# Performance work log

Hardware: AMD Instinct MI355X
Metric: run time of the kernel (lower is better)

Reference implementation:

```python
import jax, jax.numpy as jnp
import numpy as np

E, S, Q, NN_NODES, R = 2048, 256, 25, 36, 15
H = 128  # MLP hidden width


def setup_inputs() -> dict:
    key = jax.random.key(0)
    ks = jax.random.split(key, 16)
    g = lambda k, shape, scale=1.0: (jax.random.normal(k, shape, dtype=jnp.float32) * scale)
    inp = {
        "nodes": g(ks[0], (E, NN_NODES, 2)),
        "W1": g(ks[1], (2, H), 1.0 / np.sqrt(2.0)),
        "b1": jnp.zeros((H,), jnp.float32),
        "W2": g(ks[2], (H, H), 1.0 / np.sqrt(H)),
        "b2": jnp.zeros((H,), jnp.float32),
        "W3": g(ks[3], (H, H), 1.0 / np.sqrt(H)),
        "b3": jnp.zeros((H,), jnp.float32),
        "W4": g(ks[4], (H, 1), 1.0 / np.sqrt(H)),
        "b4": jnp.zeros((1,), jnp.float32),
        # 2nd-derivative interpolation matrices of the inter basis B at the
        # sub-element quadrature points (shared across big elements).
        "Ixx": g(ks[5], (S, Q, NN_NODES), 0.1),
        "Iyy": g(ks[6], (S, Q, NN_NODES), 0.1),
        # per-big-element 2x2 Hessian change-of-coordinates map (B_DD_inter)
        "B_DD": g(ks[7], (E, 2, 2)),
        "w_quad": jax.random.uniform(ks[8], (Q,), dtype=jnp.float32),
        # test-function values at quadrature points (b.Base)
        "Base": g(ks[9], (Q, R)),
        # per-sub-element Jacobians and precomputed RHS projections F_total
        "J": jax.random.uniform(ks[10], (E, S), dtype=jnp.float32),
        "F": g(ks[11], (E, S, R)),
    }
    return inp


def _mlp(x, W1, b1, W2, b2, W3, b3, W4, b4):
    h = jnp.tanh(x @ W1 + b1)
    h = jnp.tanh(h @ W2 + b2)
    h = jnp.tanh(h @ W3 + b3)
    return h @ W4 + b4


def reference(nodes, W1, b1, W2, b2, W3, b3, W4, b4,
              Ixx, Iyy, B_DD, w_quad, Base, J, F):
    # NN evaluated once per big element at its interpolation nodes: [E, n_nodes]
    ev = _mlp(nodes.reshape(-1, 2), W1, b1, W2, b2, W3, b3, W4, b4)
    ev = ev.reshape(E, NN_NODES)
    d2x = jnp.einsum("sqn,en->esq", Ixx, ev)
    d2y = jnp.einsum("sqn,en->esq", Iyy, ev)
    grad_second = jnp.stack([d2x, d2y], axis=2)           # [E,S,2,Q]
    # B_DD_inter @ grad_second^T, per big element
    grad_second = jnp.einsum("eij,esjq->esiq", B_DD, grad_second)
    integrand_1 = grad_second.sum(axis=2)                 # [E,S,Q]
    # u_NN_el[r] = -J * sum_q w[q] * Base[q,r] * integrand_1[q]
    u_el = -J[:, :, None] * jnp.einsum("q,qr,esq->esr", w_quad, Base, integrand_1)
    res = u_el - F                                        # [E,S,R]
    # loss_element = mean over test functions, summed over all (big, sub) elements
    return jnp.sum(jnp.mean(jnp.square(res), axis=-1))
```

## Files before the change

### kernel.cpp

```cpp
#include <hip/hip_runtime.h>

#define EN 2048
#define SN 256
#define QN 25
#define NNODES 36
#define RN 15
#define HN 128
#define KP 96
#define NTOT (SN * RN)

typedef __attribute__((ext_vector_type(8))) short short8;
typedef __attribute__((ext_vector_type(4))) float f32x4;
typedef __attribute__((ext_vector_type(2))) unsigned int uint2v;

__device__ __forceinline__ unsigned short f2bf(float f) {
    unsigned int u = __float_as_uint(f);
    u += 0x7fffu + ((u >> 16) & 1u);
    return (unsigned short)(u >> 16);
}
__device__ __forceinline__ float bf2f(unsigned short h) {
    return __uint_as_float(((unsigned int)h) << 16);
}
__device__ __forceinline__ float fast_tanh(float x) {
    float xs = x * 2.885390082f;
    xs = fminf(fmaxf(xs, -60.f), 60.f);
    float e = __builtin_amdgcn_exp2f(xs);
    float r = __builtin_amdgcn_rcpf(e + 1.f);
    return fmaf(-2.f, r, 1.f);
}

__device__ __forceinline__ void load_W(const float* __restrict__ W,
                                       unsigned short (*Ws)[136], int t)
{
    const int n = t & 127;
    const int h = t >> 7;
    #pragma unroll
    for (int kk = 0; kk < 16; kk++) {
        const int k0 = (kk * 2 + h) * 4;
        const float a0 = W[(k0 + 0) * HN + n];
        const float a1 = W[(k0 + 1) * HN + n];
        const float a2 = W[(k0 + 2) * HN + n];
        const float a3 = W[(k0 + 3) * HN + n];
        uint2v pk;
        pk[0] = (unsigned)f2bf(a0) | ((unsigned)f2bf(a1) << 16);
        pk[1] = (unsigned)f2bf(a2) | ((unsigned)f2bf(a3) << 16);
        *(uint2v*)&Ws[n][k0] = pk;
    }
}

__device__ __forceinline__ void mfma_layer(unsigned short (*Hs)[136],
                                           const unsigned short (*Ws)[136],
                                           const float* __restrict__ bias,
                                           int wv, int rowA, int quad)
{
    const int r0 = wv * 32;
    short8 afrag[2][4];
    #pragma unroll
    for (int rt = 0; rt < 2; rt++)
        #pragma unroll
        for (int kt = 0; kt < 4; kt++)
            afrag[rt][kt] = *(const short8*)&Hs[r0 + rt * 16 + rowA][kt * 32 + quad * 8];

    f32x4 acc[2][8];
    const f32x4 zero = {0.f, 0.f, 0.f, 0.f};
    #pragma unroll
    for (int rt = 0; rt < 2; rt++)
        #pragma unroll
        for (int nt = 0; nt < 8; nt++) acc[rt][nt] = zero;

    #pragma unroll
    for (int nt = 0; nt < 8; nt++) {
        #pragma unroll
        for (int kt = 0; kt < 4; kt++) {
            const short8 bfrag = *(const short8*)&Ws[nt * 16 + rowA][kt * 32 + quad * 8];
            acc[0][nt] = __builtin_amdgcn_mfma_f32_16x16x32_bf16(afrag[0][kt], bfrag, acc[0][nt], 0, 0, 0);
            acc[1][nt] = __builtin_amdgcn_mfma_f32_16x16x32_bf16(afrag[1][kt], bfrag, acc[1][nt], 0, 0, 0);
        }
    }
    #pragma unroll
    for (int nt = 0; nt < 8; nt++) {
        const int col = nt * 16 + rowA;
        const float bv = bias[col];
        #pragma unroll
        for (int rt = 0; rt < 2; rt++) {
            #pragma unroll
            for (int rg = 0; rg < 4; rg++) {
                const float v = fast_tanh(acc[rt][nt][rg] + bv);
                Hs[r0 + rt * 16 + quad * 4 + rg][col] = f2bf(v);
            }
        }
    }
}

#define MLP_BLOCKS 576
#define MC_BLOCKS 1440

__global__ __launch_bounds__(256, 2)
void prep_kernel(const float* __restrict__ nodes,
                 const float* __restrict__ W1, const float* __restrict__ b1,
                 const float* __restrict__ W2, const float* __restrict__ b2,
                 const float* __restrict__ W3, const float* __restrict__ b3,
                 const float* __restrict__ W4, const float* __restrict__ b4,
                 const float* __restrict__ B_DD,
                 const float* __restrict__ Ixx, const float* __restrict__ Iyy,
                 const float* __restrict__ wq, const float* __restrict__ Base,
                 unsigned short* __restrict__ evcb,
                 unsigned short* __restrict__ Mcb,
                 float* __restrict__ out)
{
    __shared__ unsigned short Hs[128][136];
    __shared__ unsigned short Ws[128][136];
    __shared__ float WB[QN * 16];
    const int bid = blockIdx.x;
    const int t   = threadIdx.x;

    if (bid < MLP_BLOCKS) {
        const int lane = t & 63;
        const int wv   = t >> 6;
        const int rowA = lane & 15;
        const int quad = lane >> 4;

        {
            const int p  = t >> 1;
            const int P  = bid * 128 + p;
            const float x0 = nodes[2 * P], x1 = nodes[2 * P + 1];
            const int n0 = (t & 1) * 64;
            #pragma unroll
            for (int i = 0; i < 16; i++) {
                const int n = n0 + 4 * i;
                const float4 wa = *(const float4*)(W1 + n);
                const float4 wb = *(const float4*)(W1 + HN + n);
                const float4 bb = *(const float4*)(b1 + n);
                const float h0 = fast_tanh(fmaf(x0, wa.x, fmaf(x1, wb.x, bb.x)));
                const float h1 = fast_tanh(fmaf(x0, wa.y, fmaf(x1, wb.y, bb.y)));
                const float h2 = fast_tanh(fmaf(x0, wa.z, fmaf(x1, wb.z, bb.z)));
                const float h3 = fast_tanh(fmaf(x0, wa.w, fmaf(x1, wb.w, bb.w)));
                uint2v pk;
                pk[0] = (unsigned)f2bf(h0) | ((unsigned)f2bf(h1) << 16);
                pk[1] = (unsigned)f2bf(h2) | ((unsigned)f2bf(h3) << 16);
                *(uint2v*)&Hs[p][n] = pk;
            }
        }
        load_W(W2, Ws, t);
        __syncthreads();
        mfma_layer(Hs, Ws, b2, wv, rowA, quad);
        __syncthreads();
        load_W(W3, Ws, t);
        __syncthreads();
        mfma_layer(Hs, Ws, b3, wv, rowA, quad);
        {
            const int p  = t >> 1;
            const int k0 = (t & 1) * 64;
            float d = 0.f;
            #pragma unroll
            for (int i = 0; i < 8; i++) {
                const short8 h = *(const short8*)&Hs[p][k0 + 8 * i];
                const float4 wA = *(const float4*)(W4 + k0 + 8 * i);
                const float4 wB = *(const float4*)(W4 + k0 + 8 * i + 4);
                d = fmaf(bf2f((unsigned short)h[0]), wA.x, d);
                d = fmaf(bf2f((unsigned short)h[1]), wA.y, d);
                d = fmaf(bf2f((unsigned short)h[2]), wA.z, d);
                d = fmaf(bf2f((unsigned short)h[3]), wA.w, d);
                d = fmaf(bf2f((unsigned short)h[4]), wB.x, d);
                d = fmaf(bf2f((unsigned short)h[5]), wB.y, d);
                d = fmaf(bf2f((unsigned short)h[6]), wB.z, d);
                d = fmaf(bf2f((unsigned short)h[7]), wB.w, d);
            }
            d += __shfl_xor(d, 1, 64);
            if ((t & 1) == 0) {
                const float ev = d + b4[0];
                const int P  = bid * 128 + p;
                const int e  = P / NNODES;
                const int ne = P - e * NNODES;
                const float c0 = B_DD[4 * e + 0] + B_DD[4 * e + 2];
                const float c1 = B_DD[4 * e + 1] + B_DD[4 * e + 3];
                evcb[e * KP + ne]          = f2bf(c0 * ev);
                evcb[e * KP + NNODES + ne] = f2bf(c1 * ev);
                if (ne < KP - 2 * NNODES)
                    evcb[e * KP + 2 * NNODES + ne] = 0;
            }
        }
    } else {
        if (bid == MLP_BLOCKS && t == 0) out[0] = 0.f;
        for (int i = t; i < QN * 16; i += 256) {
            const int q = i >> 4, r = i & 15;
            if (r < RN) WB[i] = wq[q] * Base[q * RN + r];
        }
        __syncthreads();
        const int o = (bid - MLP_BLOCKS) * 256 + t;
        const int c = o % KP;
        const int n = o / KP;
        if (c >= 2 * NNODES) { Mcb[o] = 0; return; }
        const int r = n % RN;
        const int s = n / RN;
        const float* __restrict__ I = (c < NNODES) ? Ixx : Iyy;
        const int cn = (c < NNODES) ? c : (c - NNODES);
        float a0 = 0.f, a1 = 0.f;
        #pragma unroll
        for (int q = 0; q < QN - 1; q += 2) {
            a0 = fmaf(WB[q * 16 + r],       I[(s * QN + q) * NNODES + cn],     a0);
            a1 = fmaf(WB[(q + 1) * 16 + r], I[(s * QN + q + 1) * NNODES + cn], a1);
        }
        a0 = fmaf(WB[(QN - 1) * 16 + r], I[(s * QN + QN - 1) * NNODES + cn], a0);
        Mcb[o] = f2bf(a0 + a1);
    }
}

__global__ __launch_bounds__(256, 4)
void loss_kernel(const unsigned short* __restrict__ evcb,
                 const unsigned short* __restrict__ Mcb,
                 const float* __restrict__ J, const float* __restrict__ F,
                 float* __restrict__ out)
{
    const int t    = threadIdx.x;
    const int lane = t & 63;
    const int wv   = t >> 6;
    const int rowA = lane & 15;
    const int quad = lane >> 4;
    const int m0 = (blockIdx.x & 31) * 64;
    const int n0 = (blockIdx.x >> 5) * 128 + wv * 32;

    f32x4 acc[4][2];
    const f32x4 zero = {0.f, 0.f, 0.f, 0.f};
    #pragma unroll
    for (int mt = 0; mt < 4; mt++)
        #pragma unroll
        for (int nt = 0; nt < 2; nt++) acc[mt][nt] = zero;

    #pragma unroll
    for (int kt = 0; kt < 3; kt++) {
        short8 a[4], b[2];
        #pragma unroll
        for (int mt = 0; mt < 4; mt++)
            a[mt] = *(const short8*)&evcb[(m0 + mt * 16 + rowA) * KP + kt * 32 + quad * 8];
        #pragma unroll
        for (int nt = 0; nt < 2; nt++)
            b[nt] = *(const short8*)&Mcb[(n0 + nt * 16 + rowA) * KP + kt * 32 + quad * 8];
        #pragma unroll
        for (int mt = 0; mt < 4; mt++)
            #pragma unroll
            for (int nt = 0; nt < 2; nt++)
                acc[mt][nt] = __builtin_amdgcn_mfma_f32_16x16x32_bf16(a[mt], b[nt], acc[mt][nt], 0, 0, 0);
    }

    float total = 0.f;
    #pragma unroll
    for (int nt = 0; nt < 2; nt++) {
        const int n = n0 + nt * 16 + rowA;
        const int s = (n * 34953) >> 19;
        #pragma unroll
        for (int mt = 0; mt < 4; mt++) {
            const int eb = m0 + mt * 16 + quad * 4;
            #pragma unroll
            for (int rg = 0; rg < 4; rg++) {
                const int e = eb + rg;
                const float Jv = J[e * SN + s];
                const float Fv = F[e * NTOT + n];
                const float d  = acc[mt][nt][rg];
                const float res = fmaf(-Jv, d, -Fv);
                total = fmaf(res, res, total);
            }
        }
    }
    total *= (1.f / (float)RN);

    #pragma unroll
    for (int off = 32; off; off >>= 1)
        total += __shfl_down(total, off, 64);
    __shared__ float wsum[4];
    if (lane == 0) wsum[wv] = total;
    __syncthreads();
    if (t == 0) atomicAdd(out, (wsum[0] + wsum[1]) + (wsum[2] + wsum[3]));
}

extern "C" void kernel_launch(void* const* d_in, const int* in_sizes, int n_in,
                              void* d_out, int out_size, void* d_ws, size_t ws_size,
                              hipStream_t stream)
{
    (void)in_sizes; (void)n_in; (void)out_size; (void)ws_size;
    const float* nodes = (const float*)d_in[0];
    const float* W1   = (const float*)d_in[1];
    const float* b1   = (const float*)d_in[2];
    const float* W2   = (const float*)d_in[3];
    const float* b2   = (const float*)d_in[4];
    const float* W3   = (const float*)d_in[5];
    const float* b3   = (const float*)d_in[6];
    const float* W4   = (const float*)d_in[7];
    const float* b4   = (const float*)d_in[8];
    const float* Ixx  = (const float*)d_in[9];
    const float* Iyy  = (const float*)d_in[10];
    const float* B_DD = (const float*)d_in[11];
    const float* wq   = (const float*)d_in[12];
    const float* Base = (const float*)d_in[13];
    const float* J    = (const float*)d_in[14];
    const float* F    = (const float*)d_in[15];
    float* out = (float*)d_out;
    unsigned short* evcb = (unsigned short*)d_ws;
    unsigned short* Mcb  = (unsigned short*)((char*)d_ws + EN * KP * 2);

    prep_kernel<<<MLP_BLOCKS + MC_BLOCKS, 256, 0, stream>>>(
        nodes, W1, b1, W2, b2, W3, b3, W4, b4, B_DD, Ixx, Iyy, wq, Base,
        evcb, Mcb, out);
    loss_kernel<<<32 * 30, 256, 0, stream>>>(evcb, Mcb, J, F, out);
}
```

Before: 154.1 us.

## Stage Ixx/Iyy per sub-element in LDS and prefetch F before MFMA loop

The M-matrix construction now uses one block per sub-element instead of one thread per output. Each block stages that sub-element's Ixx/Iyy slices into shared memory and reuses them across all test functions, rather than rereading them from global memory for every output. The loss kernel also loads its F values into registers before the MFMA loop so their latency overlaps the matrix compute. The cost is fewer M-construction blocks with more serial work each, and higher register pressure in the loss kernel.

```diff
diff --git a/kernel.cpp b/kernel.cpp
--- a/kernel.cpp
+++ b/kernel.cpp
@@ -93,7 +93,7 @@
 }
 
 #define MLP_BLOCKS 576
-#define MC_BLOCKS 1440
+#define MC_BLOCKS  SN
 
 __global__ __launch_bounds__(256, 2)
 void prep_kernel(const float* __restrict__ nodes,
@@ -181,28 +181,38 @@
             }
         }
     } else {
-        if (bid == MLP_BLOCKS && t == 0) out[0] = 0.f;
+        const int s = bid - MLP_BLOCKS;
+        if (s == 0 && t == 0) out[0] = 0.f;
+        float* I_lds = (float*)&Hs[0][0];
         for (int i = t; i < QN * 16; i += 256) {
             const int q = i >> 4, r = i & 15;
             if (r < RN) WB[i] = wq[q] * Base[q * RN + r];
         }
+        const float* __restrict__ Ia = Ixx + (size_t)s * (QN * NNODES);
+        const float* __restrict__ Ib = Iyy + (size_t)s * (QN * NNODES);
+        for (int i = t; i < QN * NNODES; i += 256) {
+            I_lds[i]               = Ia[i];
+            I_lds[QN * NNODES + i] = Ib[i];
+        }
         __syncthreads();
-        const int o = (bid - MLP_BLOCKS) * 256 + t;
-        const int c = o % KP;
-        const int n = o / KP;
-        if (c >= 2 * NNODES) { Mcb[o] = 0; return; }
-        const int r = n % RN;
-        const int s = n / RN;
-        const float* __restrict__ I = (c < NNODES) ? Ixx : Iyy;
-        const int cn = (c < NNODES) ? c : (c - NNODES);
-        float a0 = 0.f, a1 = 0.f;
-        #pragma unroll
-        for (int q = 0; q < QN - 1; q += 2) {
-            a0 = fmaf(WB[q * 16 + r],       I[(s * QN + q) * NNODES + cn],     a0);
-            a1 = fmaf(WB[(q + 1) * 16 + r], I[(s * QN + q + 1) * NNODES + cn], a1);
-        }
-        a0 = fmaf(WB[(QN - 1) * 16 + r], I[(s * QN + QN - 1) * NNODES + cn], a0);
-        Mcb[o] = f2bf(a0 + a1);
+        for (int o = t; o < RN * KP; o += 256) {
+            const int c = o % KP;
+            const int r = o / KP;
+            float v = 0.f;
+            if (c < 2 * NNODES) {
+                const float* __restrict__ Ip =
+                    I_lds + ((c < NNODES) ? c : (QN * NNODES + c - NNODES));
+                float a0 = 0.f, a1 = 0.f;
+                #pragma unroll
+                for (int q = 0; q < QN - 1; q += 2) {
+                    a0 = fmaf(WB[q * 16 + r],       Ip[q * NNODES],       a0);
+                    a1 = fmaf(WB[(q + 1) * 16 + r], Ip[(q + 1) * NNODES], a1);
+                }
+                a0 = fmaf(WB[(QN - 1) * 16 + r], Ip[(QN - 1) * NNODES], a0);
+                v = a0 + a1;
+            }
+            Mcb[((size_t)s * RN + r) * KP + c] = f2bf(v);
+        }
     }
 }
 
@@ -220,6 +230,17 @@
     const int m0 = (blockIdx.x & 31) * 64;
     const int n0 = (blockIdx.x >> 5) * 128 + wv * 32;
 
+    float Fv[2][16];
+    #pragma unroll
+    for (int nt = 0; nt < 2; nt++) {
+        const int n = n0 + nt * 16 + rowA;
+        #pragma unroll
+        for (int mt = 0; mt < 4; mt++)
+            #pragma unroll
+            for (int rg = 0; rg < 4; rg++)
+                Fv[nt][mt * 4 + rg] = F[(size_t)(m0 + mt * 16 + quad * 4 + rg) * NTOT + n];
+    }
+
     f32x4 acc[4][2];
     const f32x4 zero = {0.f, 0.f, 0.f, 0.f};
     #pragma unroll
@@ -232,10 +253,10 @@
         short8 a[4], b[2];
         #pragma unroll
         for (int mt = 0; mt < 4; mt++)
-            a[mt] = *(const short8*)&evcb[(m0 + mt * 16 + rowA) * KP + kt * 32 + quad * 8];
+            a[mt] = *(const short8*)&evcb[(size_t)(m0 + mt * 16 + rowA) * KP + kt * 32 + quad * 8];
         #pragma unroll
         for (int nt = 0; nt < 2; nt++)
-            b[nt] = *(const short8*)&Mcb[(n0 + nt * 16 + rowA) * KP + kt * 32 + quad * 8];
+            b[nt] = *(const short8*)&Mcb[(size_t)(n0 + nt * 16 + rowA) * KP + kt * 32 + quad * 8];
         #pragma unroll
         for (int mt = 0; mt < 4; mt++)
             #pragma unroll
@@ -253,11 +274,9 @@
             const int eb = m0 + mt * 16 + quad * 4;
             #pragma unroll
             for (int rg = 0; rg < 4; rg++) {
-                const int e = eb + rg;
-                const float Jv = J[e * SN + s];
-                const float Fv = F[e * NTOT + n];
+                const float Jv = J[(size_t)(eb + rg) * SN + s];
                 const float d  = acc[mt][nt][rg];
-                const float res = fmaf(-Jv, d, -Fv);
+                const float res = fmaf(-Jv, d, -Fv[nt][mt * 4 + rg]);
                 total = fmaf(res, res, total);
             }
         }
```

New measurement: 143.9 us. 1.07x faster.
